# Kernel tuning notes

Measured on AMD Instinct MI355X. Metric: run time of the kernel, lower is better.

## Reference

```python
import jax, jax.numpy as jnp
import numpy as np

N_VERTICES = 100000
N_JOINTS = 24
N_BETAS = 300
PARENTS = [0, 0, 0, 0, 1, 2, 3, 4, 5, 6, 7, 8, 9, 9, 9, 12, 13, 14, 16, 17, 18, 19, 20, 21]


def rodrigues(r):
    """r: [N,1,3] axis-angle -> [N,3,3] rotation matrices.

    Original adds N(0,1e-8) noise before the norm purely to avoid 0/0; we use a
    deterministic epsilon inside the sqrt instead (same math up to ~1e-8).
    """
    theta = jnp.sqrt(jnp.sum(r * r, axis=(1, 2), keepdims=True) + 1e-16)  # [N,1,1]
    r_hat = r / theta                                                      # [N,1,3]
    cos = jnp.cos(theta)
    sin = jnp.sin(theta)
    x, y, z = r_hat[:, 0, 0], r_hat[:, 0, 1], r_hat[:, 0, 2]
    zero = jnp.zeros_like(x)
    m = jnp.stack([zero, -z, y, z, zero, -x, -y, x, zero], axis=1).reshape(-1, 3, 3)
    dot = jnp.einsum('nia,nib->nab', r_hat, r_hat)  # outer product r_hat^T r_hat
    eye = jnp.eye(3, dtype=r.dtype)
    return cos * eye + (1.0 - cos) * dot + sin * m


def _with_zeros(R3, t):
    # [3,3],[3] -> [4,4] homogeneous transform
    top = jnp.concatenate([R3, t[:, None]], axis=1)              # [3,4]
    bottom = jnp.array([[0.0, 0.0, 0.0, 1.0]], dtype=R3.dtype)
    return jnp.concatenate([top, bottom], axis=0)


def smpl_forward(beta, pose, v_template, J_regressor, skin_weights, shapedirs, posedirs):
    dtype = v_template.dtype
    # shape blendshapes: [V,3,K] . [K] -> [V,3]
    v_shaped = jnp.einsum('vdk,k->vd', shapedirs, beta) + v_template
    J = J_regressor @ v_shaped                                   # [24,3]

    pose_cube = pose.reshape(-1, 1, 3)                           # [24,1,3]
    R_cube_big = rodrigues(pose_cube)                            # [24,3,3]

    # pose blendshapes
    lrotmin = (R_cube_big[1:] - jnp.eye(3, dtype=dtype)).reshape(-1)   # [207]
    v_posed = v_shaped + jnp.einsum('vdp,p->vd', posedirs, lrotmin)    # [V,3]

    # kinematic chain (fixed 24-step sequential dependency)
    Gs = [_with_zeros(R_cube_big[0], J[0])]
    for i in range(1, N_JOINTS):
        j = PARENTS[i]
        Gs.append(Gs[j] @ _with_zeros(R_cube_big[i], J[i] - J[j]))
    G = jnp.stack(Gs)                                            # [24,4,4]

    # remove rest-pose joint locations: G - pad(G @ [J;0])
    J_h = jnp.concatenate([J, jnp.zeros((N_JOINTS, 1), dtype=dtype)], axis=1)  # [24,4]
    RJ = jnp.einsum('jab,jb->ja', G, J_h)                        # [24,4]
    G = G - jnp.pad(RJ[:, :, None], ((0, 0), (0, 0), (3, 0)))    # subtract into last column

    # linear blend skinning
    T = jnp.einsum('vj,jab->vab', skin_weights, G)               # [V,4,4]
    rest_h = jnp.pad(v_posed, ((0, 0), (0, 1)), constant_values=1.0)  # [V,4]
    v = jnp.einsum('vab,vb->va', T, rest_h)                      # [V,4]
    return v[:, :3]


def setup_inputs() -> dict:
    key = jax.random.key(0)
    ks = jax.random.split(key, 7)
    beta = jax.random.normal(ks[0], (N_BETAS,), dtype=jnp.float32)
    pose = jax.random.normal(ks[1], (N_JOINTS * 3,), dtype=jnp.float32)
    v_template = jax.random.normal(ks[2], (N_VERTICES, 3), dtype=jnp.float32)
    # NonNegUnitSum(axis=1) constraints -> nonnegative rows summing to 1
    Jr = jax.random.uniform(ks[3], (N_JOINTS, N_VERTICES), dtype=jnp.float32)
    J_regressor = Jr / jnp.sum(Jr, axis=1, keepdims=True)
    w = jax.random.uniform(ks[4], (N_VERTICES, N_JOINTS), dtype=jnp.float32)
    skin_weights = w / jnp.sum(w, axis=1, keepdims=True)
    shapedirs = 0.01 * jax.random.normal(ks[5], (N_VERTICES, 3, N_BETAS), dtype=jnp.float32)
    posedirs = 0.01 * jax.random.normal(ks[6], (N_VERTICES, 3, (N_JOINTS - 1) * 9), dtype=jnp.float32)
    return {'beta': beta, 'pose': pose, 'v_template': v_template,
            'J_regressor': J_regressor, 'skin_weights': skin_weights,
            'shapedirs': shapedirs, 'posedirs': posedirs}


def reference(beta, pose, v_template, J_regressor, skin_weights, shapedirs, posedirs):
    return smpl_forward(beta, pose, v_template, J_regressor, skin_weights, shapedirs, posedirs)
```

## Files before the change

kernel.cpp:

```cpp
#include <hip/hip_runtime.h>
#include <math.h>

#define N_V 100000
#define N_J 24
#define N_BETAS 300
#define N_POSE 207
#define JSPLIT 25

typedef float f4 __attribute__((ext_vector_type(4)));

__constant__ int c_parents[N_J] = {0,0,0,0,1,2,3,4,5,6,7,8,9,9,9,12,13,14,16,17,18,19,20,21};

__global__ void k_rodrigues(const float* __restrict__ pose,
                            float* __restrict__ ws_R,
                            float* __restrict__ ws_lrot) {
    __shared__ float Rsh[N_J][9];
    int t = threadIdx.x;
    if (t < N_J) {
        float x = pose[t*3+0], y = pose[t*3+1], z = pose[t*3+2];
        float th = sqrtf(x*x + y*y + z*z + 1e-16f);
        float inv = 1.0f / th;
        float rx = x*inv, ry = y*inv, rz = z*inv;
        float c = cosf(th), s = sinf(th), o = 1.0f - c;
        float R[9];
        R[0] = c + o*rx*rx;      R[1] = o*rx*ry - s*rz;  R[2] = o*rx*rz + s*ry;
        R[3] = o*ry*rx + s*rz;   R[4] = c + o*ry*ry;     R[5] = o*ry*rz - s*rx;
        R[6] = o*rz*rx - s*ry;   R[7] = o*rz*ry + s*rx;  R[8] = c + o*rz*rz;
        #pragma unroll
        for (int i = 0; i < 9; ++i) { Rsh[t][i] = R[i]; ws_R[t*9+i] = R[i]; }
    }
    __syncthreads();
    for (int i = t; i < N_POSE; i += blockDim.x) {
        int j = i / 9 + 1, e = i % 9;
        float v = Rsh[j][e];
        if (e == 0 || e == 4 || e == 8) v -= 1.0f;
        ws_lrot[i] = v;
    }
}

__global__ __launch_bounds__(256) void k_vertex(
        const float* __restrict__ shapedirs, const float* __restrict__ posedirs,
        const float* __restrict__ v_template, const float* __restrict__ beta,
        const float* __restrict__ lrot,
        float* __restrict__ vs, float* __restrict__ vp) {
    int lane = threadIdx.x & 63;
    int wave = threadIdx.x >> 6;
    int vb = blockIdx.x * 16 + wave * 4;

    f4 bv[4];
    #pragma unroll
    for (int it = 0; it < 4; ++it) {
        int i = lane + it * 64;
        int d = (i >= 150) ? 2 : ((i >= 75) ? 1 : 0);
        int k4 = i - d * 75;
        if (it < 3 || i < 225) bv[it] = ((const f4*)beta)[k4];
        else                   bv[it] = (f4){0.f, 0.f, 0.f, 0.f};
    }
    float lr[10];
    #pragma unroll
    for (int it = 0; it < 10; ++it) {
        int i = lane + it * 64;
        int d = (i >= 414) ? 2 : ((i >= 207) ? 1 : 0);
        int p = i - d * 207;
        lr[it] = (it < 9 || i < 621) ? lrot[p] : 0.f;
    }

    #pragma unroll 2
    for (int u = 0; u < 4; ++u) {
        int v = vb + u;
        const f4*    sb = (const f4*)(shapedirs + (size_t)v * 900);
        const float* pb = posedirs + (size_t)v * 621;

        f4 s0 = __builtin_nontemporal_load(sb + lane);
        f4 s1 = __builtin_nontemporal_load(sb + lane + 64);
        f4 s2 = __builtin_nontemporal_load(sb + lane + 128);
        f4 s3 = (lane < 33) ? __builtin_nontemporal_load(sb + lane + 192)
                            : (f4){0.f, 0.f, 0.f, 0.f};
        float q0 = __builtin_nontemporal_load(pb + lane);
        float q1 = __builtin_nontemporal_load(pb + lane +  64);
        float q2 = __builtin_nontemporal_load(pb + lane + 128);
        float q3 = __builtin_nontemporal_load(pb + lane + 192);
        float q4 = __builtin_nontemporal_load(pb + lane + 256);
        float q5 = __builtin_nontemporal_load(pb + lane + 320);
        float q6 = __builtin_nontemporal_load(pb + lane + 384);
        float q7 = __builtin_nontemporal_load(pb + lane + 448);
        float q8 = __builtin_nontemporal_load(pb + lane + 512);
        float q9 = (lane < 45) ? __builtin_nontemporal_load(pb + lane + 576) : 0.f;

        float a0 = 0.f, a1 = 0.f, a2 = 0.f;
        float p0 = 0.f, p1 = 0.f, p2 = 0.f;

        float c0 = s0.x*bv[0].x + s0.y*bv[0].y + s0.z*bv[0].z + s0.w*bv[0].w;
        float c1 = s1.x*bv[1].x + s1.y*bv[1].y + s1.z*bv[1].z + s1.w*bv[1].w;
        float c2 = s2.x*bv[2].x + s2.y*bv[2].y + s2.z*bv[2].z + s2.w*bv[2].w;
        float c3 = s3.x*bv[3].x + s3.y*bv[3].y + s3.z*bv[3].z + s3.w*bv[3].w;
        a0 += c0;
        if (lane < 11) a0 += c1; else a1 += c1;
        if (lane < 22) a1 += c2; else a2 += c2;
        a2 += c3;

        p0 += q0 * lr[0];
        p0 += q1 * lr[1];
        p0 += q2 * lr[2];
        { float c = q3 * lr[3]; if (lane < 15) p0 += c; else p1 += c; }
        p1 += q4 * lr[4];
        p1 += q5 * lr[5];
        { float c = q6 * lr[6]; if (lane < 30) p1 += c; else p2 += c; }
        p2 += q7 * lr[7];
        p2 += q8 * lr[8];
        p2 += q9 * lr[9];

        #pragma unroll
        for (int off = 1; off <= 4; off <<= 1) {
            a0 += __shfl_xor(a0, off); a1 += __shfl_xor(a1, off); a2 += __shfl_xor(a2, off);
            p0 += __shfl_xor(p0, off); p1 += __shfl_xor(p1, off); p2 += __shfl_xor(p2, off);
        }
        int j = lane & 7;
        float val = a0;
        val = (j == 1) ? a1 : val;
        val = (j == 2) ? a2 : val;
        val = (j == 3) ? p0 : val;
        val = (j == 4) ? p1 : val;
        val = (j == 5) ? p2 : val;
        val += __shfl_xor(val, 8);
        val += __shfl_xor(val, 16);
        val += __shfl_xor(val, 32);
        float pj = __shfl(val, lane + 3);

        if (lane < 3) {
            float vsd = val + v_template[(size_t)v*3 + lane];
            vs[lane * N_V + v] = vsd;
            vp[lane * N_V + v] = vsd + pj;
        }
    }
}

__global__ __launch_bounds__(256) void k_jreg(const float* __restrict__ Jr,
                                              const float* __restrict__ vs,
                                              float* __restrict__ jpart) {
    int j = blockIdx.x / JSPLIT;
    int s = blockIdx.x % JSPLIT;
    const int chunk4 = (N_V / JSPLIT) / 4;
    int b4 = s * chunk4;
    int t = threadIdx.x;
    const f4* row = (const f4*)(Jr + (size_t)j * N_V);
    const f4* X = (const f4*)(vs);
    const f4* Y = (const f4*)(vs + N_V);
    const f4* Z = (const f4*)(vs + 2 * N_V);
    float a0 = 0.f, a1 = 0.f, a2 = 0.f;
    for (int i = b4 + t; i < b4 + chunk4; i += 256) {
        f4 w = row[i];
        f4 x = X[i], y = Y[i], z = Z[i];
        a0 += w.x*x.x + w.y*x.y + w.z*x.z + w.w*x.w;
        a1 += w.x*y.x + w.y*y.y + w.z*y.z + w.w*y.w;
        a2 += w.x*z.x + w.y*z.y + w.z*z.z + w.w*z.w;
    }
    #pragma unroll
    for (int off = 32; off; off >>= 1) {
        a0 += __shfl_xor(a0, off); a1 += __shfl_xor(a1, off); a2 += __shfl_xor(a2, off);
    }
    __shared__ float red[4][3];
    int wave = t >> 6, lane = t & 63;
    if (lane == 0) { red[wave][0] = a0; red[wave][1] = a1; red[wave][2] = a2; }
    __syncthreads();
    if (t == 0) {
        jpart[(j*JSPLIT+s)*3+0] = red[0][0]+red[1][0]+red[2][0]+red[3][0];
        jpart[(j*JSPLIT+s)*3+1] = red[0][1]+red[1][1]+red[2][1]+red[3][1];
        jpart[(j*JSPLIT+s)*3+2] = red[0][2]+red[1][2]+red[2][2]+red[3][2];
    }
}

__global__ void k_chain(const float* __restrict__ jpart,
                        const float* __restrict__ ws_R,
                        float* __restrict__ ws_G) {
    __shared__ float J[N_J][3];
    __shared__ float G[N_J][16];
    int t = threadIdx.x;
    for (int i = t; i < N_J * 3; i += 64) {
        int j = i / 3, d = i % 3;
        float s = 0.f;
        for (int k = 0; k < JSPLIT; ++k) s += jpart[(j*JSPLIT+k)*3 + d];
        J[j][d] = s;
    }
    __syncthreads();
    if (t < 16) {
        int a = t / 4, b = t % 4;
        float g;
        if (a < 3) g = (b < 3) ? ws_R[a*3 + b] : J[0][a];
        else       g = (b == 3) ? 1.f : 0.f;
        G[0][t] = g;
    }
    __syncthreads();
    for (int i = 1; i < N_J; ++i) {
        int p = c_parents[i];
        if (t < 16) {
            int a = t / 4, b = t % 4;
            float acc = 0.f;
            #pragma unroll
            for (int k = 0; k < 4; ++k) {
                float Ak;
                if (k < 3) Ak = (b < 3) ? ws_R[i*9 + k*3 + b] : (J[i][k] - J[p][k]);
                else       Ak = (b == 3) ? 1.f : 0.f;
                acc += G[p][a*4 + k] * Ak;
            }
            G[i][t] = acc;
        }
        __syncthreads();
    }
    for (int i = t; i < N_J * 12; i += 64) {
        int j = i / 12, r = i % 12, a = r / 4, b = r % 4;
        float g = G[j][a*4 + b];
        if (b == 3)
            g -= G[j][a*4+0]*J[j][0] + G[j][a*4+1]*J[j][1] + G[j][a*4+2]*J[j][2];
        ws_G[i] = g;
    }
}

__global__ __launch_bounds__(256) void k_skin(const float* __restrict__ w,
                                              const float* __restrict__ ws_G,
                                              const float* __restrict__ vp,
                                              float* __restrict__ out) {
    __shared__ float G[N_J * 12];
    int t = threadIdx.x;
    for (int i = t; i < N_J * 12; i += 256) G[i] = ws_G[i];
    __syncthreads();
    int v = blockIdx.x * 256 + t;
    if (v >= N_V) return;
    float T[12];
    #pragma unroll
    for (int r = 0; r < 12; ++r) T[r] = 0.f;
    const f4* wv = (const f4*)(w + (size_t)v * 24);
    #pragma unroll
    for (int q = 0; q < 6; ++q) {
        f4 ww = __builtin_nontemporal_load(wv + q);
        float wj[4] = {ww.x, ww.y, ww.z, ww.w};
        #pragma unroll
        for (int jj = 0; jj < 4; ++jj) {
            const float* g = &G[(q*4 + jj) * 12];
            #pragma unroll
            for (int r = 0; r < 12; ++r) T[r] += wj[jj] * g[r];
        }
    }
    float px = vp[v], py = vp[N_V + v], pz = vp[2*N_V + v];
    out[v*3+0] = T[0]*px + T[1]*py + T[2]*pz  + T[3];
    out[v*3+1] = T[4]*px + T[5]*py + T[6]*pz  + T[7];
    out[v*3+2] = T[8]*px + T[9]*py + T[10]*pz + T[11];
}

extern "C" void kernel_launch(void* const* d_in, const int* in_sizes, int n_in,
                              void* d_out, int out_size, void* d_ws, size_t ws_size,
                              hipStream_t stream) {
    const float* beta       = (const float*)d_in[0];
    const float* pose       = (const float*)d_in[1];
    const float* v_template = (const float*)d_in[2];
    const float* Jr         = (const float*)d_in[3];
    const float* skin_w     = (const float*)d_in[4];
    const float* shapedirs  = (const float*)d_in[5];
    const float* posedirs   = (const float*)d_in[6];
    float* out = (float*)d_out;

    float* ws      = (float*)d_ws;
    float* ws_R    = ws;
    float* ws_lrot = ws + 256;
    float* ws_vs   = ws + 512;
    float* ws_vp   = ws + 512 + 3*N_V;
    float* ws_jp   = ws + 512 + 6*N_V;
    float* ws_G    = ws + 512 + 6*N_V + 2048;

    k_rodrigues<<<1, 256, 0, stream>>>(pose, ws_R, ws_lrot);
    k_vertex<<<N_V / 16, 256, 0, stream>>>(shapedirs, posedirs, v_template,
                                           beta, ws_lrot, ws_vs, ws_vp);
    k_jreg<<<N_J * JSPLIT, 256, 0, stream>>>(Jr, ws_vs, ws_jp);
    k_chain<<<1, 64, 0, stream>>>(ws_jp, ws_R, ws_G);
    k_skin<<<(N_V + 255) / 256, 256, 0, stream>>>(skin_w, ws_G, ws_vp, out);
}
```

Before: 130.4 us.

## Fuse joint regression into vertex kernel and kinematic chain into skinning

Computes the per-block J_regressor partial sums inside the vertex kernel, so v_shaped is no longer written to and reread from memory. A small reduce kernel then sums the per-block partials. The kinematic chain is recomputed redundantly in every skinning block, which removes one launch. Each block now handles 32 vertices instead of 16. The risks are strided, uncoalesced reads of Jr (24 rows read per vertex), a sequential 24-step chain with syncs repeated in every skin block, and a larger partial buffer.

```diff
diff --git a/kernel.cpp b/kernel.cpp
--- a/kernel.cpp
+++ b/kernel.cpp
@@ -5,7 +5,8 @@
 #define N_J 24
 #define N_BETAS 300
 #define N_POSE 207
-#define JSPLIT 25
+#define WPB 32
+#define NBLK (N_V / WPB)
 
 typedef float f4 __attribute__((ext_vector_type(4)));
 
@@ -41,11 +42,11 @@
 __global__ __launch_bounds__(256) void k_vertex(
         const float* __restrict__ shapedirs, const float* __restrict__ posedirs,
         const float* __restrict__ v_template, const float* __restrict__ beta,
-        const float* __restrict__ lrot,
-        float* __restrict__ vs, float* __restrict__ vp) {
+        const float* __restrict__ lrot, const float* __restrict__ Jr,
+        float* __restrict__ vp, float* __restrict__ jpart) {
     int lane = threadIdx.x & 63;
     int wave = threadIdx.x >> 6;
-    int vb = blockIdx.x * 16 + wave * 4;
+    int vb = blockIdx.x * WPB + wave * 8;
 
     f4 bv[4];
     #pragma unroll
@@ -65,8 +66,10 @@
         lr[it] = (it < 9 || i < 621) ? lrot[p] : 0.f;
     }
 
+    float jp0 = 0.f, jp1 = 0.f, jp2 = 0.f;
+
     #pragma unroll 2
-    for (int u = 0; u < 4; ++u) {
+    for (int u = 0; u < 8; ++u) {
         int v = vb + u;
         const f4*    sb = (const f4*)(shapedirs + (size_t)v * 900);
         const float* pb = posedirs + (size_t)v * 621;
@@ -127,61 +130,56 @@
         val += __shfl_xor(val, 32);
         float pj = __shfl(val, lane + 3);
 
+        float vsd = val + ((lane < 3) ? v_template[(size_t)v*3 + lane] : 0.f);
+        float vx = __shfl(vsd, 0), vy = __shfl(vsd, 1), vz = __shfl(vsd, 2);
+        if (lane < N_J) {
+            float w = Jr[(size_t)lane * N_V + v];
+            jp0 += w * vx; jp1 += w * vy; jp2 += w * vz;
+        }
         if (lane < 3) {
-            float vsd = val + v_template[(size_t)v*3 + lane];
-            vs[lane * N_V + v] = vsd;
             vp[lane * N_V + v] = vsd + pj;
         }
     }
-}
-
-__global__ __launch_bounds__(256) void k_jreg(const float* __restrict__ Jr,
-                                              const float* __restrict__ vs,
-                                              float* __restrict__ jpart) {
-    int j = blockIdx.x / JSPLIT;
-    int s = blockIdx.x % JSPLIT;
-    const int chunk4 = (N_V / JSPLIT) / 4;
-    int b4 = s * chunk4;
-    int t = threadIdx.x;
-    const f4* row = (const f4*)(Jr + (size_t)j * N_V);
-    const f4* X = (const f4*)(vs);
-    const f4* Y = (const f4*)(vs + N_V);
-    const f4* Z = (const f4*)(vs + 2 * N_V);
-    float a0 = 0.f, a1 = 0.f, a2 = 0.f;
-    for (int i = b4 + t; i < b4 + chunk4; i += 256) {
-        f4 w = row[i];
-        f4 x = X[i], y = Y[i], z = Z[i];
-        a0 += w.x*x.x + w.y*x.y + w.z*x.z + w.w*x.w;
-        a1 += w.x*y.x + w.y*y.y + w.z*y.z + w.w*y.w;
-        a2 += w.x*z.x + w.y*z.y + w.z*z.z + w.w*z.w;
-    }
-    #pragma unroll
-    for (int off = 32; off; off >>= 1) {
-        a0 += __shfl_xor(a0, off); a1 += __shfl_xor(a1, off); a2 += __shfl_xor(a2, off);
-    }
-    __shared__ float red[4][3];
+
+    __shared__ float jsh[4][N_J][3];
+    if (lane < N_J) {
+        jsh[wave][lane][0] = jp0; jsh[wave][lane][1] = jp1; jsh[wave][lane][2] = jp2;
+    }
+    __syncthreads();
+    int t = threadIdx.x;
+    if (t < N_J * 3) {
+        int j = t / 3, d = t % 3;
+        float s = jsh[0][j][d] + jsh[1][j][d] + jsh[2][j][d] + jsh[3][j][d];
+        jpart[(size_t)t * NBLK + blockIdx.x] = s;
+    }
+}
+
+__global__ __launch_bounds__(256) void k_jreduce(const float* __restrict__ jpart,
+                                                 float* __restrict__ Jg) {
+    int c = blockIdx.x;
+    const float* col = jpart + (size_t)c * NBLK;
+    int t = threadIdx.x;
+    float s = 0.f;
+    for (int i = t; i < NBLK; i += 256) s += col[i];
+    #pragma unroll
+    for (int off = 32; off; off >>= 1) s += __shfl_xor(s, off);
+    __shared__ float red[4];
     int wave = t >> 6, lane = t & 63;
-    if (lane == 0) { red[wave][0] = a0; red[wave][1] = a1; red[wave][2] = a2; }
-    __syncthreads();
-    if (t == 0) {
-        jpart[(j*JSPLIT+s)*3+0] = red[0][0]+red[1][0]+red[2][0]+red[3][0];
-        jpart[(j*JSPLIT+s)*3+1] = red[0][1]+red[1][1]+red[2][1]+red[3][1];
-        jpart[(j*JSPLIT+s)*3+2] = red[0][2]+red[1][2]+red[2][2]+red[3][2];
-    }
-}
-
-__global__ void k_chain(const float* __restrict__ jpart,
-                        const float* __restrict__ ws_R,
-                        float* __restrict__ ws_G) {
+    if (lane == 0) red[wave] = s;
+    __syncthreads();
+    if (t == 0) Jg[c] = red[0] + red[1] + red[2] + red[3];
+}
+
+__global__ __launch_bounds__(256) void k_skin(const float* __restrict__ w,
+                                              const float* __restrict__ Jg,
+                                              const float* __restrict__ ws_R,
+                                              const float* __restrict__ vp,
+                                              float* __restrict__ out) {
     __shared__ float J[N_J][3];
     __shared__ float G[N_J][16];
-    int t = threadIdx.x;
-    for (int i = t; i < N_J * 3; i += 64) {
-        int j = i / 3, d = i % 3;
-        float s = 0.f;
-        for (int k = 0; k < JSPLIT; ++k) s += jpart[(j*JSPLIT+k)*3 + d];
-        J[j][d] = s;
-    }
+    __shared__ float Gp[N_J * 12];
+    int t = threadIdx.x;
+    if (t < N_J * 3) J[t/3][t%3] = Jg[t];
     __syncthreads();
     if (t < 16) {
         int a = t / 4, b = t % 4;
@@ -207,23 +205,15 @@
         }
         __syncthreads();
     }
-    for (int i = t; i < N_J * 12; i += 64) {
+    for (int i = t; i < N_J * 12; i += 256) {
         int j = i / 12, r = i % 12, a = r / 4, b = r % 4;
         float g = G[j][a*4 + b];
         if (b == 3)
             g -= G[j][a*4+0]*J[j][0] + G[j][a*4+1]*J[j][1] + G[j][a*4+2]*J[j][2];
-        ws_G[i] = g;
-    }
-}
-
-__global__ __launch_bounds__(256) void k_skin(const float* __restrict__ w,
-                                              const float* __restrict__ ws_G,
-                                              const float* __restrict__ vp,
-                                              float* __restrict__ out) {
-    __shared__ float G[N_J * 12];
-    int t = threadIdx.x;
-    for (int i = t; i < N_J * 12; i += 256) G[i] = ws_G[i];
-    __syncthreads();
+        Gp[i] = g;
+    }
+    __syncthreads();
+
     int v = blockIdx.x * 256 + t;
     if (v >= N_V) return;
     float T[12];
@@ -236,7 +226,7 @@
         float wj[4] = {ww.x, ww.y, ww.z, ww.w};
         #pragma unroll
         for (int jj = 0; jj < 4; ++jj) {
-            const float* g = &G[(q*4 + jj) * 12];
+            const float* g = &Gp[(q*4 + jj) * 12];
             #pragma unroll
             for (int r = 0; r < 12; ++r) T[r] += wj[jj] * g[r];
         }
@@ -262,15 +252,13 @@
     float* ws      = (float*)d_ws;
     float* ws_R    = ws;
     float* ws_lrot = ws + 256;
-    float* ws_vs   = ws + 512;
-    float* ws_vp   = ws + 512 + 3*N_V;
-    float* ws_jp   = ws + 512 + 6*N_V;
-    float* ws_G    = ws + 512 + 6*N_V + 2048;
+    float* ws_vp   = ws + 512;
+    float* ws_jp   = ws + 512 + 3*N_V;
+    float* ws_J    = ws + 512 + 3*N_V + 225024;
 
     k_rodrigues<<<1, 256, 0, stream>>>(pose, ws_R, ws_lrot);
-    k_vertex<<<N_V / 16, 256, 0, stream>>>(shapedirs, posedirs, v_template,
-                                           beta, ws_lrot, ws_vs, ws_vp);
-    k_jreg<<<N_J * JSPLIT, 256, 0, stream>>>(Jr, ws_vs, ws_jp);
-    k_chain<<<1, 64, 0, stream>>>(ws_jp, ws_R, ws_G);
-    k_skin<<<(N_V + 255) / 256, 256, 0, stream>>>(skin_w, ws_G, ws_vp, out);
-}
+    k_vertex<<<NBLK, 256, 0, stream>>>(shapedirs, posedirs, v_template,
+                                       beta, ws_lrot, Jr, ws_vp, ws_jp);
+    k_jreduce<<<N_J * 3, 256, 0, stream>>>(ws_jp, ws_J);
+    k_skin<<<(N_V + 255) / 256, 256, 0, stream>>>(skin_w, ws_J, ws_R, ws_vp, out);
+}
```

After: 144.9 us. 1.11x slower.

## Vectorize posedirs loads and fuse kinematic chain into skinning kernel

Applied to the files above, without the earlier changes.

The posedirs dot product in k_vertex now loads 16-byte f4 chunks per lane instead of ten scalar loads, with the lrot coefficients prearranged to match and boundary lanes split across the x/y/z partial sums. The single-block k_chain kernel is removed, and every k_skin block now recomputes J and the 24-joint chain itself in shared memory. This saves a kernel launch and a global round trip for G, but adds the serial 23-step chain with its barriers to every one of about 391 skinning blocks. The vectorized loads also drop the nontemporal hint, and their 16-byte alignment is not guaranteed because each vertex row is 621 floats long.

```diff
diff --git a/kernel.cpp b/kernel.cpp
--- a/kernel.cpp
+++ b/kernel.cpp
@@ -56,14 +56,11 @@
         if (it < 3 || i < 225) bv[it] = ((const f4*)beta)[k4];
         else                   bv[it] = (f4){0.f, 0.f, 0.f, 0.f};
     }
-    float lr[10];
-    #pragma unroll
-    for (int it = 0; it < 10; ++it) {
-        int i = lane + it * 64;
-        int d = (i >= 414) ? 2 : ((i >= 207) ? 1 : 0);
-        int p = i - d * 207;
-        lr[it] = (it < 9 || i < 621) ? lrot[p] : 0.f;
-    }
+    int f0 = 4 * lane;
+    f4 lrc0 = { lrot[(f0+0)%207], lrot[(f0+1)%207], lrot[(f0+2)%207], lrot[(f0+3)%207] };
+    f4 lrc1 = { lrot[(f0+256)%207], lrot[(f0+257)%207], lrot[(f0+258)%207], lrot[(f0+259)%207] };
+    f4 lrc2 = { lrot[(f0+512)%207], lrot[(f0+513)%207], lrot[(f0+514)%207], lrot[(f0+515)%207] };
+    float tc = lrot[206];
 
     #pragma unroll 2
     for (int u = 0; u < 4; ++u) {
@@ -76,16 +73,11 @@
         f4 s2 = __builtin_nontemporal_load(sb + lane + 128);
         f4 s3 = (lane < 33) ? __builtin_nontemporal_load(sb + lane + 192)
                             : (f4){0.f, 0.f, 0.f, 0.f};
-        float q0 = __builtin_nontemporal_load(pb + lane);
-        float q1 = __builtin_nontemporal_load(pb + lane +  64);
-        float q2 = __builtin_nontemporal_load(pb + lane + 128);
-        float q3 = __builtin_nontemporal_load(pb + lane + 192);
-        float q4 = __builtin_nontemporal_load(pb + lane + 256);
-        float q5 = __builtin_nontemporal_load(pb + lane + 320);
-        float q6 = __builtin_nontemporal_load(pb + lane + 384);
-        float q7 = __builtin_nontemporal_load(pb + lane + 448);
-        float q8 = __builtin_nontemporal_load(pb + lane + 512);
-        float q9 = (lane < 45) ? __builtin_nontemporal_load(pb + lane + 576) : 0.f;
+        f4 x0, x1, x2 = (f4){0.f, 0.f, 0.f, 0.f};
+        __builtin_memcpy(&x0, pb + f0, 16);
+        __builtin_memcpy(&x1, pb + f0 + 256, 16);
+        if (lane < 27) __builtin_memcpy(&x2, pb + f0 + 512, 16);
+        float tail = (lane == 27) ? pb[620] : 0.f;
 
         float a0 = 0.f, a1 = 0.f, a2 = 0.f;
         float p0 = 0.f, p1 = 0.f, p2 = 0.f;
@@ -99,16 +91,16 @@
         if (lane < 22) a1 += c2; else a2 += c2;
         a2 += c3;
 
-        p0 += q0 * lr[0];
-        p0 += q1 * lr[1];
-        p0 += q2 * lr[2];
-        { float c = q3 * lr[3]; if (lane < 15) p0 += c; else p1 += c; }
-        p1 += q4 * lr[4];
-        p1 += q5 * lr[5];
-        { float c = q6 * lr[6]; if (lane < 30) p1 += c; else p2 += c; }
-        p2 += q7 * lr[7];
-        p2 += q8 * lr[8];
-        p2 += q9 * lr[9];
+        float d0 = x0.x*lrc0.x + x0.y*lrc0.y + x0.z*lrc0.z + x0.w*lrc0.w;
+        float d1 = x1.x*lrc1.x + x1.y*lrc1.y + x1.z*lrc1.z + x1.w*lrc1.w;
+        float d2 = x2.x*lrc2.x + x2.y*lrc2.y + x2.z*lrc2.z + x2.w*lrc2.w;
+        if (lane < 51)       p0 += d0;
+        else if (lane == 51) { float hi = x0.w * lrc0.w; p0 += d0 - hi; p1 += hi; }
+        else                 p1 += d0;
+        if (lane < 39)       p1 += d1;
+        else if (lane == 39) { float hi = x1.z*lrc1.z + x1.w*lrc1.w; p1 += d1 - hi; p2 += hi; }
+        else                 p2 += d1;
+        p2 += d2 + tail * tc;
 
         #pragma unroll
         for (int off = 1; off <= 4; off <<= 1) {
@@ -170,15 +162,19 @@
     }
 }
 
-__global__ void k_chain(const float* __restrict__ jpart,
-                        const float* __restrict__ ws_R,
-                        float* __restrict__ ws_G) {
+__global__ __launch_bounds__(256) void k_skin(const float* __restrict__ w,
+                                              const float* __restrict__ jpart,
+                                              const float* __restrict__ ws_R,
+                                              const float* __restrict__ vp,
+                                              float* __restrict__ out) {
     __shared__ float J[N_J][3];
     __shared__ float G[N_J][16];
+    __shared__ float Gp[N_J * 12];
     int t = threadIdx.x;
-    for (int i = t; i < N_J * 3; i += 64) {
-        int j = i / 3, d = i % 3;
+    if (t < N_J * 3) {
+        int j = t / 3, d = t % 3;
         float s = 0.f;
+        #pragma unroll
         for (int k = 0; k < JSPLIT; ++k) s += jpart[(j*JSPLIT+k)*3 + d];
         J[j][d] = s;
     }
@@ -207,23 +203,15 @@
         }
         __syncthreads();
     }
-    for (int i = t; i < N_J * 12; i += 64) {
+    for (int i = t; i < N_J * 12; i += 256) {
         int j = i / 12, r = i % 12, a = r / 4, b = r % 4;
         float g = G[j][a*4 + b];
         if (b == 3)
             g -= G[j][a*4+0]*J[j][0] + G[j][a*4+1]*J[j][1] + G[j][a*4+2]*J[j][2];
-        ws_G[i] = g;
-    }
-}
-
-__global__ __launch_bounds__(256) void k_skin(const float* __restrict__ w,
-                                              const float* __restrict__ ws_G,
-                                              const float* __restrict__ vp,
-                                              float* __restrict__ out) {
-    __shared__ float G[N_J * 12];
-    int t = threadIdx.x;
-    for (int i = t; i < N_J * 12; i += 256) G[i] = ws_G[i];
-    __syncthreads();
+        Gp[i] = g;
+    }
+    __syncthreads();
+
     int v = blockIdx.x * 256 + t;
     if (v >= N_V) return;
     float T[12];
@@ -236,7 +224,7 @@
         float wj[4] = {ww.x, ww.y, ww.z, ww.w};
         #pragma unroll
         for (int jj = 0; jj < 4; ++jj) {
-            const float* g = &G[(q*4 + jj) * 12];
+            const float* g = &Gp[(q*4 + jj) * 12];
             #pragma unroll
             for (int r = 0; r < 12; ++r) T[r] += wj[jj] * g[r];
         }
@@ -265,12 +253,10 @@
     float* ws_vs   = ws + 512;
     float* ws_vp   = ws + 512 + 3*N_V;
     float* ws_jp   = ws + 512 + 6*N_V;
-    float* ws_G    = ws + 512 + 6*N_V + 2048;
 
     k_rodrigues<<<1, 256, 0, stream>>>(pose, ws_R, ws_lrot);
     k_vertex<<<N_V / 16, 256, 0, stream>>>(shapedirs, posedirs, v_template,
                                            beta, ws_lrot, ws_vs, ws_vp);
     k_jreg<<<N_J * JSPLIT, 256, 0, stream>>>(Jr, ws_vs, ws_jp);
-    k_chain<<<1, 64, 0, stream>>>(ws_jp, ws_R, ws_G);
-    k_skin<<<(N_V + 255) / 256, 256, 0, stream>>>(skin_w, ws_G, ws_vp, out);
-}
+    k_skin<<<(N_V + 255) / 256, 256, 0, stream>>>(skin_w, ws_jp, ws_R, ws_vp, out);
+}
```

Result: faster. 123.3 us (-5.4%).
